# Optimization experiments

Measured on AMD Instinct MI355X. Metric: run time of the kernel, lower is better.

## Reference

```python
import jax, jax.numpy as jnp
import numpy as np

N_TX, N_ACC, E = 500000, 100000, 1000000
D_TX, D_ACC, H = 64, 32, 64


def setup_inputs() -> dict:
    key = jax.random.key(0)
    ks = jax.random.split(key, 16)
    s = 0.05
    return {
        "x_tx": jax.random.normal(ks[0], (N_TX, D_TX), jnp.float32),
        "x_acc": jax.random.normal(ks[1], (N_ACC, D_ACC), jnp.float32),
        "pays_src": jax.random.randint(ks[2], (E,), 0, N_ACC),
        "pays_dst": jax.random.randint(ks[3], (E,), 0, N_TX),
        "rev_src": jax.random.randint(ks[4], (E,), 0, N_TX),
        "rev_dst": jax.random.randint(ks[5], (E,), 0, N_ACC),
        # SAGEConv for ('account','pays','transaction'): lin_l: D_ACC->H (bias), lin_r: D_TX->H (no bias)
        "Wl_pays": jax.random.normal(ks[6], (D_ACC, H), jnp.float32) * s,
        "bl_pays": jnp.zeros((H,), jnp.float32),
        "Wr_pays": jax.random.normal(ks[7], (D_TX, H), jnp.float32) * s,
        # SAGEConv for ('transaction','rev_pays','account'): lin_l: D_TX->H, lin_r: D_ACC->H
        "Wl_rev": jax.random.normal(ks[8], (D_TX, H), jnp.float32) * s,
        "bl_rev": jnp.zeros((H,), jnp.float32),
        "Wr_rev": jax.random.normal(ks[9], (D_ACC, H), jnp.float32) * s,
        # output head Linear(H, 1)
        "W_out": jax.random.normal(ks[10], (H, 1), jnp.float32) * s,
        "b_out": jnp.zeros((1,), jnp.float32),
    }


def _segment_mean(msg, dst, n_dst):
    # scatter-mean: sum per dst node / clamped degree (isolated nodes -> 0)
    s = jax.ops.segment_sum(msg, dst, num_segments=n_dst)
    c = jax.ops.segment_sum(jnp.ones((dst.shape[0], 1), msg.dtype), dst, num_segments=n_dst)
    return s / jnp.maximum(c, 1.0)


def _sage(x_src, x_dst, src, dst, Wl, bl, Wr):
    agg = _segment_mean(x_src[src], dst, x_dst.shape[0])  # [n_dst, d_src]
    return agg @ Wl + bl + x_dst @ Wr  # [n_dst, H]


def reference(x_tx, x_acc, pays_src, pays_dst, rev_src, rev_dst,
              Wl_pays, bl_pays, Wr_pays, Wl_rev, bl_rev, Wr_rev, W_out, b_out):
    # HeteroConv: each dst node type receives exactly one edge type here, so aggr='mean' is identity
    h_tx = _sage(x_acc, x_tx, pays_src, pays_dst, Wl_pays, bl_pays, Wr_pays)
    h_acc = _sage(x_tx, x_acc, rev_src, rev_dst, Wl_rev, bl_rev, Wr_rev)
    tx_x = jax.nn.relu(h_tx)
    _ = jax.nn.relu(h_acc)  # computed by the module but unused downstream
    logits = (tx_x @ W_out + b_out)[:, 0]
    return logits, tx_x
```

## Files before the change

kernel.cpp:

```cpp
#include <hip/hip_runtime.h>

#define N_TX   500000
#define N_ACC  100000
#define E_CNT  1000000
#define D_TX   64
#define D_ACC  32
#define H_DIM  64

#define SCAN_B    256
#define SCAN_I    8
#define SCAN_TILE (SCAN_B * SCAN_I)
#define NSCAN_BLOCKS ((N_TX + SCAN_TILE - 1) / SCAN_TILE)


__global__ __launch_bounds__(256) void hist_kernel(
    const int* __restrict__ dst, int* __restrict__ cnt) {
    int e = blockIdx.x * blockDim.x + threadIdx.x;
    if (e < E_CNT) atomicAdd(&cnt[dst[e]], 1);
}

__global__ __launch_bounds__(SCAN_B) void scan1_kernel(
    const int* __restrict__ cnt, int* __restrict__ offs, int* __restrict__ bsum) {
    __shared__ int lds[SCAN_B];
    int base = blockIdx.x * SCAN_TILE + threadIdx.x * SCAN_I;
    int v[SCAN_I];
    int tsum = 0;
#pragma unroll
    for (int i = 0; i < SCAN_I; ++i) {
        int idx = base + i;
        v[i] = (idx < N_TX) ? cnt[idx] : 0;
        tsum += v[i];
    }
    lds[threadIdx.x] = tsum;
    __syncthreads();
    for (int off = 1; off < SCAN_B; off <<= 1) {
        int a = 0;
        if ((int)threadIdx.x >= off) a = lds[threadIdx.x - off];
        __syncthreads();
        lds[threadIdx.x] += a;
        __syncthreads();
    }
    int texcl = lds[threadIdx.x] - tsum;
    if (threadIdx.x == SCAN_B - 1) bsum[blockIdx.x] = lds[SCAN_B - 1];
    int run = texcl;
#pragma unroll
    for (int i = 0; i < SCAN_I; ++i) {
        int idx = base + i;
        if (idx < N_TX) offs[idx] = run;
        run += v[i];
    }
}

__global__ __launch_bounds__(256) void scan2_kernel(int* __restrict__ bsum, int nb) {
    __shared__ int lds[256];
    int t = threadIdx.x;
    int v = (t < nb) ? bsum[t] : 0;
    lds[t] = v;
    __syncthreads();
    for (int off = 1; off < 256; off <<= 1) {
        int a = 0;
        if (t >= off) a = lds[t - off];
        __syncthreads();
        lds[t] += a;
        __syncthreads();
    }
    if (t < nb) bsum[t] = lds[t] - v;
}

__global__ __launch_bounds__(256) void finalize_kernel(
    int* __restrict__ offs, int* __restrict__ cursors, const int* __restrict__ bsum) {
    int i = blockIdx.x * blockDim.x + threadIdx.x;
    if (i < N_TX) {
        int f = offs[i] + bsum[i / SCAN_TILE];
        offs[i] = f;
        cursors[i] = f;
    }
}

__global__ __launch_bounds__(256) void fill_kernel(
    const int* __restrict__ src, const int* __restrict__ dst,
    int* __restrict__ cursors, int* __restrict__ eidx) {
    int e = blockIdx.x * blockDim.x + threadIdx.x;
    if (e < E_CNT) {
        int d = dst[e];
        int p = atomicAdd(&cursors[d], 1);
        eidx[p] = src[e];
    }
}

__global__ __launch_bounds__(256, 4) void row_kernel(
    const float* __restrict__ x_tx,
    const float* __restrict__ x_acc,
    const int*   __restrict__ offs,
    const int*   __restrict__ cnt,
    const int*   __restrict__ eidx,
    const float* __restrict__ Wl,
    const float* __restrict__ bl,
    const float* __restrict__ Wr,
    const float* __restrict__ Wout,
    const float* __restrict__ bout,
    float*       __restrict__ logits,
    float*       __restrict__ txx,
    int total_waves) {
    int lane = threadIdx.x & 63;
    int wave = (blockIdx.x * blockDim.x + threadIdx.x) >> 6;

    float wl[D_ACC];
#pragma unroll
    for (int k = 0; k < D_ACC; ++k) wl[k] = Wl[k * H_DIM + lane];
    float wr[D_TX];
#pragma unroll
    for (int k = 0; k < D_TX; ++k) wr[k] = Wr[k * H_DIM + lane];
    float wo = Wout[lane];
    float b  = bl[lane];
    float bo = bout[0];

    for (int row = wave; row < N_TX; row += total_waves) {
        int urow = __builtin_amdgcn_readfirstlane(row);

        const float4* xr = (const float4*)(x_tx + (size_t)urow * D_TX);
        float a0 = 0.f, a1 = 0.f, a2 = 0.f, a3 = 0.f;
#pragma unroll
        for (int q = 0; q < 16; ++q) {
            float4 v = xr[q];
            a0 = fmaf(v.x, wr[4 * q + 0], a0);
            a1 = fmaf(v.y, wr[4 * q + 1], a1);
            a2 = fmaf(v.z, wr[4 * q + 2], a2);
            a3 = fmaf(v.w, wr[4 * q + 3], a3);
        }
        float hx = (a0 + a1) + (a2 + a3) + b;

        int deg = __builtin_amdgcn_readfirstlane(cnt[urow]);
        int off = __builtin_amdgcn_readfirstlane(offs[urow]);
        float g0 = 0.f, g1 = 0.f, g2 = 0.f, g3 = 0.f;
        for (int e = 0; e < deg; ++e) {
            int s = __builtin_amdgcn_readfirstlane(eidx[off + e]);
            const float4* ar = (const float4*)(x_acc + (size_t)s * D_ACC);
#pragma unroll
            for (int q = 0; q < 8; ++q) {
                float4 v = ar[q];
                g0 = fmaf(v.x, wl[4 * q + 0], g0);
                g1 = fmaf(v.y, wl[4 * q + 1], g1);
                g2 = fmaf(v.z, wl[4 * q + 2], g2);
                g3 = fmaf(v.w, wl[4 * q + 3], g3);
            }
        }
        float ha  = (g0 + g1) + (g2 + g3);
        float inv = 1.0f / (float)(deg > 0 ? deg : 1);

        float h = fmaf(ha, inv, hx);
        float r = fmaxf(h, 0.0f);
        txx[(size_t)urow * H_DIM + lane] = r;

        float p = r * wo;
#pragma unroll
        for (int s = 32; s > 0; s >>= 1) p += __shfl_down(p, s);
        if (lane == 0) logits[urow] = p + bo;
    }
}

extern "C" void kernel_launch(void* const* d_in, const int* in_sizes, int n_in,
                              void* d_out, int out_size, void* d_ws, size_t ws_size,
                              hipStream_t stream) {
    const float* x_tx     = (const float*)d_in[0];
    const float* x_acc    = (const float*)d_in[1];
    const int*   pays_src = (const int*)d_in[2];
    const int*   pays_dst = (const int*)d_in[3];
    const float* Wl   = (const float*)d_in[6];
    const float* bl   = (const float*)d_in[7];
    const float* Wr   = (const float*)d_in[8];
    const float* Wout = (const float*)d_in[12];
    const float* bout = (const float*)d_in[13];

    float* out    = (float*)d_out;
    float* logits = out;
    float* txx    = out + N_TX;

    int* cnt     = (int*)d_ws;
    int* offs    = cnt + N_TX;
    int* cursors = offs + N_TX;
    int* bsum    = cursors + N_TX;
    int* eidx    = bsum + 1024;

    hipMemsetAsync(cnt, 0, (size_t)N_TX * sizeof(int), stream);

    hist_kernel<<<(E_CNT + 255) / 256, 256, 0, stream>>>(pays_dst, cnt);
    scan1_kernel<<<NSCAN_BLOCKS, SCAN_B, 0, stream>>>(cnt, offs, bsum);
    scan2_kernel<<<1, 256, 0, stream>>>(bsum, NSCAN_BLOCKS);
    finalize_kernel<<<(N_TX + 255) / 256, 256, 0, stream>>>(offs, cursors, bsum);
    fill_kernel<<<(E_CNT + 255) / 256, 256, 0, stream>>>(pays_src, pays_dst, cursors, eidx);

    const int blocks = 2048;
    row_kernel<<<blocks, 256, 0, stream>>>(
        x_tx, x_acc, offs, cnt, eidx, Wl, bl, Wr, Wout, bout,
        logits, txx, blocks * 4);
}
```

Measured before the change: 724.3 us.

## Pre-transform account features by Wl, then gather transformed rows per edge

Adds a kernel that computes x_acc @ Wl once for every account into a workspace buffer. The row kernel then gathers one 64-float transformed row per edge, with one coalesced load per lane, instead of 32 floats followed by 32 FMAs per lane. Rows are now assigned to waves in contiguous chunks rather than strided, and the first gather is software-prefetched ahead of the x_tx GEMV. The cost is an extra 25.6 MB transform write and twice the bytes per edge gather, in exchange for much less per-edge ALU work and fewer registers.

```diff
diff --git a/kernel.cpp b/kernel.cpp
--- a/kernel.cpp
+++ b/kernel.cpp
@@ -88,73 +88,95 @@
     }
 }
 
+__global__ __launch_bounds__(256, 4) void acc_transform_kernel(
+    const float* __restrict__ x_acc, const float* __restrict__ Wl,
+    float* __restrict__ y, int rows_per_wave) {
+    int lane = threadIdx.x & 63;
+    int wave = (blockIdx.x * blockDim.x + threadIdx.x) >> 6;
+    float wl[D_ACC];
+#pragma unroll
+    for (int k = 0; k < D_ACC; ++k) wl[k] = Wl[k * H_DIM + lane];
+    int r0 = wave * rows_per_wave;
+    int r1 = min(r0 + rows_per_wave, N_ACC);
+    for (int row = r0; row < r1; ++row) {
+        int urow = __builtin_amdgcn_readfirstlane(row);
+        const float4* xr = (const float4*)(x_acc + (size_t)urow * D_ACC);
+        float a0 = 0.f, a1 = 0.f, a2 = 0.f, a3 = 0.f;
+#pragma unroll
+        for (int q = 0; q < 8; ++q) {
+            float4 v = xr[q];
+            a0 = fmaf(v.x, wl[4 * q + 0], a0);
+            a1 = fmaf(v.y, wl[4 * q + 1], a1);
+            a2 = fmaf(v.z, wl[4 * q + 2], a2);
+            a3 = fmaf(v.w, wl[4 * q + 3], a3);
+        }
+        y[(size_t)urow * H_DIM + lane] = (a0 + a1) + (a2 + a3);
+    }
+}
+
 __global__ __launch_bounds__(256, 4) void row_kernel(
     const float* __restrict__ x_tx,
-    const float* __restrict__ x_acc,
+    const float* __restrict__ y,
     const int*   __restrict__ offs,
     const int*   __restrict__ cnt,
     const int*   __restrict__ eidx,
-    const float* __restrict__ Wl,
+    const float* __restrict__ Wr,
     const float* __restrict__ bl,
-    const float* __restrict__ Wr,
     const float* __restrict__ Wout,
     const float* __restrict__ bout,
     float*       __restrict__ logits,
     float*       __restrict__ txx,
-    int total_waves) {
+    int rows_per_wave) {
     int lane = threadIdx.x & 63;
     int wave = (blockIdx.x * blockDim.x + threadIdx.x) >> 6;
 
-    float wl[D_ACC];
-#pragma unroll
-    for (int k = 0; k < D_ACC; ++k) wl[k] = Wl[k * H_DIM + lane];
     float wr[D_TX];
 #pragma unroll
     for (int k = 0; k < D_TX; ++k) wr[k] = Wr[k * H_DIM + lane];
+    float b  = bl[lane];
     float wo = Wout[lane];
-    float b  = bl[lane];
     float bo = bout[0];
 
-    for (int row = wave; row < N_TX; row += total_waves) {
+    int r0 = wave * rows_per_wave;
+    int r1 = min(r0 + rows_per_wave, N_TX);
+    for (int row = r0; row < r1; ++row) {
         int urow = __builtin_amdgcn_readfirstlane(row);
+        int deg = __builtin_amdgcn_readfirstlane(cnt[urow]);
+        int off = __builtin_amdgcn_readfirstlane(offs[urow]);
+
+        float g = 0.f, v = 0.f;
+        if (deg > 0) {
+            int s0 = __builtin_amdgcn_readfirstlane(eidx[off]);
+            v = y[(size_t)s0 * H_DIM + lane];
+        }
 
         const float4* xr = (const float4*)(x_tx + (size_t)urow * D_TX);
         float a0 = 0.f, a1 = 0.f, a2 = 0.f, a3 = 0.f;
 #pragma unroll
         for (int q = 0; q < 16; ++q) {
-            float4 v = xr[q];
-            a0 = fmaf(v.x, wr[4 * q + 0], a0);
-            a1 = fmaf(v.y, wr[4 * q + 1], a1);
-            a2 = fmaf(v.z, wr[4 * q + 2], a2);
-            a3 = fmaf(v.w, wr[4 * q + 3], a3);
-        }
-        float hx = (a0 + a1) + (a2 + a3) + b;
-
-        int deg = __builtin_amdgcn_readfirstlane(cnt[urow]);
-        int off = __builtin_amdgcn_readfirstlane(offs[urow]);
-        float g0 = 0.f, g1 = 0.f, g2 = 0.f, g3 = 0.f;
-        for (int e = 0; e < deg; ++e) {
-            int s = __builtin_amdgcn_readfirstlane(eidx[off + e]);
-            const float4* ar = (const float4*)(x_acc + (size_t)s * D_ACC);
-#pragma unroll
-            for (int q = 0; q < 8; ++q) {
-                float4 v = ar[q];
-                g0 = fmaf(v.x, wl[4 * q + 0], g0);
-                g1 = fmaf(v.y, wl[4 * q + 1], g1);
-                g2 = fmaf(v.z, wl[4 * q + 2], g2);
-                g3 = fmaf(v.w, wl[4 * q + 3], g3);
-            }
-        }
-        float ha  = (g0 + g1) + (g2 + g3);
+            float4 xv = xr[q];
+            a0 = fmaf(xv.x, wr[4 * q + 0], a0);
+            a1 = fmaf(xv.y, wr[4 * q + 1], a1);
+            a2 = fmaf(xv.z, wr[4 * q + 2], a2);
+            a3 = fmaf(xv.w, wr[4 * q + 3], a3);
+        }
+
+        for (int e = 1; e < deg; ++e) {
+            int s2 = __builtin_amdgcn_readfirstlane(eidx[off + e]);
+            float v2 = y[(size_t)s2 * H_DIM + lane];
+            g += v;
+            v = v2;
+        }
+        if (deg > 0) g += v;
+
         float inv = 1.0f / (float)(deg > 0 ? deg : 1);
-
-        float h = fmaf(ha, inv, hx);
-        float r = fmaxf(h, 0.0f);
+        float h = ((a0 + a1) + (a2 + a3)) + b + g * inv;
+        float r = fmaxf(h, 0.f);
         txx[(size_t)urow * H_DIM + lane] = r;
 
         float p = r * wo;
 #pragma unroll
-        for (int s = 32; s > 0; s >>= 1) p += __shfl_down(p, s);
+        for (int sh = 32; sh > 0; sh >>= 1) p += __shfl_down(p, sh);
         if (lane == 0) logits[urow] = p + bo;
     }
 }
@@ -181,6 +203,7 @@
     int* cursors = offs + N_TX;
     int* bsum    = cursors + N_TX;
     int* eidx    = bsum + 1024;
+    float* y     = (float*)(eidx + E_CNT);
 
     hipMemsetAsync(cnt, 0, (size_t)N_TX * sizeof(int), stream);
 
@@ -190,8 +213,16 @@
     finalize_kernel<<<(N_TX + 255) / 256, 256, 0, stream>>>(offs, cursors, bsum);
     fill_kernel<<<(E_CNT + 255) / 256, 256, 0, stream>>>(pays_src, pays_dst, cursors, eidx);
 
-    const int blocks = 2048;
-    row_kernel<<<blocks, 256, 0, stream>>>(
-        x_tx, x_acc, offs, cnt, eidx, Wl, bl, Wr, Wout, bout,
-        logits, txx, blocks * 4);
-}
+    {
+        const int blocks = 512;
+        int rpw = (N_ACC + blocks * 4 - 1) / (blocks * 4);
+        acc_transform_kernel<<<blocks, 256, 0, stream>>>(x_acc, Wl, y, rpw);
+    }
+
+    {
+        const int blocks = 2048;
+        int rpw = (N_TX + blocks * 4 - 1) / (blocks * 4);
+        row_kernel<<<blocks, 256, 0, stream>>>(
+            x_tx, y, offs, cnt, eidx, Wr, bl, Wout, bout, logits, txx, rpw);
+    }
+}
```

Result: faster. 677.8 us (-6.4%).
